# Optimization experiments

Measured on AMD Instinct MI355X. Metric: run time of the kernel, lower is better.

## Reference

```python
import jax, jax.numpy as jnp
import numpy as np

GRID_SIZE = 5
SPLINE_ORDER = 3


def _haar_filters():
    # db1 (Haar) decomposition filters, matching wavelet.create_wavelet_filter:
    # dec_lo[::-1] = [s, s], dec_hi[::-1] = [s, -s]; rec filters are identical for Haar.
    s = np.float32(1.0 / np.sqrt(2.0))
    lo = np.array([s, s], np.float32)
    hi = np.array([s, -s], np.float32)
    # f = a.unsqueeze(0) * b.unsqueeze(1)  ->  f[p, q] = a[q] * b[p]
    def outer(a, b):
        return b[:, None] * a[None, :]
    dec = np.stack([outer(lo, lo), outer(lo, hi), outer(hi, lo), outer(hi, hi)], 0)  # (4,2,2): LL,LH,HL,HH
    return jnp.asarray(dec), jnp.asarray(dec)


def depthwise_conv5(x, w, b):
    # torch Conv2d(C, C, 5, padding='same', groups=C)
    y = jax.lax.conv_general_dilated(
        x, w, window_strides=(1, 1), padding=[(2, 2), (2, 2)],
        dimension_numbers=('NCHW', 'OIHW', 'NCHW'), feature_group_count=x.shape[1])
    return y + b[None, :, None, None]


def kan_linear(x, base_w, spline_w, scaler):
    # efficient-kan KANLinear: base SiLU linear + B-spline linear over last dim.
    in_f = x.shape[-1]
    out_f = base_w.shape[0]
    shp = x.shape
    xf = x.reshape(-1, in_f)                      # (N, in)
    h = 2.0 / GRID_SIZE                           # grid_range [-1, 1]
    grid_1d = jnp.arange(-SPLINE_ORDER, GRID_SIZE + SPLINE_ORDER + 1, dtype=xf.dtype) * h - 1.0
    grid = jnp.broadcast_to(grid_1d, (in_f, grid_1d.shape[0]))  # (in, G+2k+1)
    xe = xf[:, :, None]
    bases = ((xe >= grid[:, :-1]) & (xe < grid[:, 1:])).astype(xf.dtype)
    for k in range(1, SPLINE_ORDER + 1):
        bases = ((xe - grid[:, :-(k + 1)]) / (grid[:, k:-1] - grid[:, :-(k + 1)]) * bases[..., :-1]
                 + (grid[:, k + 1:] - xe) / (grid[:, k + 1:] - grid[:, 1:-k]) * bases[..., 1:])
    # bases: (N, in, G+k)
    base_out = jax.nn.silu(xf) @ base_w.T
    sw = spline_w * scaler[:, :, None]            # scaled_spline_weight (out, in, G+k)
    spline_out = jnp.einsum('nig,oig->no', bases, sw)
    return (base_out + spline_out).reshape(*shp[:-1], out_f)


def setup_inputs() -> dict:
    key = jax.random.key(0)
    ks = jax.random.split(key, 6)
    C, H, W, B = 32, 256, 256, 4
    in_f = C * 4  # 128
    return {
        'x': jax.random.normal(ks[0], (B, C, H, W), jnp.float32),
        'conv_w': jax.random.normal(ks[1], (C, 1, 5, 5), jnp.float32) * 0.2,
        'conv_b': jax.random.normal(ks[2], (C,), jnp.float32) * 0.02,
        'kan_base_w': jax.random.normal(ks[3], (in_f, in_f), jnp.float32) * (1.0 / np.sqrt(in_f)),
        'kan_spline_w': jax.random.normal(ks[4], (in_f, in_f, GRID_SIZE + SPLINE_ORDER), jnp.float32) * 0.1,
        'kan_spline_scaler': 1.0 + 0.1 * jax.random.normal(ks[5], (in_f, in_f), jnp.float32),
    }


def reference(x, conv_w, conv_b, kan_base_w, kan_spline_w, kan_spline_scaler):
    dec, rec = _haar_filters()
    b, c, hh, ww = x.shape
    # Level-1 skip: depthwise base_conv on full-res input
    skip = depthwise_conv5(x, conv_w, conv_b)
    # Haar wavelet transform (stride-2 non-overlapping 2x2 depthwise conv) via reshape+einsum
    x5 = x.reshape(b, c, hh // 2, 2, ww // 2, 2)
    wt = jnp.einsum('bcipjq,kpq->bckij', x5, dec)  # (b, c, 4, h/2, w/2)
    # Subband KAN over last (width) dim of 128 == in_channels*4 -> msi_kan branch
    z = kan_linear(wt, kan_base_w, kan_spline_w, kan_spline_scaler)
    # Inverse wavelet (stride-2 conv_transpose) via einsum scatter
    y = jnp.einsum('bckij,kpq->bcipjq', z, rec).reshape(b, c, hh, ww)
    return y + skip
```

## Files before the change

### kernel.cpp

```cpp
#include <hip/hip_runtime.h>
#include <hip/hip_bf16.h>

using f32x4 = __attribute__((ext_vector_type(4))) float;
using s16x8 = __attribute__((ext_vector_type(8))) short;
using u32x4 = __attribute__((ext_vector_type(4))) unsigned;

constexpr int Bn = 4, Cc = 32, Hh = 256, Ww = 256;
constexpr int H2 = 128, W2 = 128;
constexpr int NF = 128;
constexpr long NROWS = (long)Bn * Cc * 4 * H2;
constexpr int KTOT = 1152;
constexpr int KCH = 288;

__device__ __forceinline__ short f2bf(float f) {
    union { float f; unsigned u; } v; v.f = f;
    unsigned r = v.u + 0x7fffu + ((v.u >> 16) & 1u);
    return (short)(r >> 16);
}

__device__ __forceinline__ unsigned pk_bf16(float a, float b) {
    union { __hip_bfloat162 h; unsigned u; } c;
    c.h.x = __float2bfloat16(a);
    c.h.y = __float2bfloat16(b);
    return c.u;
}

__device__ __forceinline__ void gload_lds16(const void* g, void* l) {
    __builtin_amdgcn_global_load_lds(
        (const __attribute__((address_space(1))) unsigned*)g,
        (__attribute__((address_space(3))) unsigned*)l, 16, 0, 0);
}

__device__ __forceinline__ void window128(float wD, float wC, float wB, float wA,
                                          int ci, unsigned W[4]) {
    unsigned long long P = ((unsigned long long)pk_bf16(wB, wA) << 32)
                         | (unsigned long long)pk_bf16(wD, wC);
    int sh = ci * 16 - 48;
    unsigned long long sl = P << (sh & 63);
    unsigned long long sr = P >> ((-sh) & 63);
    unsigned long long lo = (sh < 0) ? sr : ((sh < 64) ? sl : 0ull);
    int shh = sh - 64;
    unsigned long long sl2 = P << (shh & 63);
    unsigned long long sr2 = P >> ((-shh) & 63);
    unsigned long long hi = (shh >= 0) ? sl2 : (((-shh) < 64) ? sr2 : 0ull);
    W[0] = (unsigned)lo; W[1] = (unsigned)(lo >> 32);
    W[2] = (unsigned)hi; W[3] = (unsigned)(hi >> 32);
}

__global__ __launch_bounds__(256) void k_wbuild(const float* __restrict__ base_w,
                                                const float* __restrict__ spline_w,
                                                const float* __restrict__ scaler,
                                                short* __restrict__ Bg) {
    int idx = blockIdx.x * 256 + threadIdx.x;
    int tile = idx >> 9;
    int r = idx & 511;
    int lane = r >> 3, q = r & 7;
    int ni = tile / 36; int rem = tile - ni * 36;
    int jg = rem / 9;   int ks = rem - jg * 9;
    int o = ni * 16 + (lane & 15);
    int kk = ks * 32 + (lane >> 4) * 8 + q;
    int g = kk >> 5, jl = kk & 31;
    int j = jg * 32 + jl;
    float v = (g == 0) ? base_w[o * NF + j]
                       : spline_w[(long)(o * NF + j) * 8 + (g - 1)] * scaler[o * NF + j];
    Bg[idx] = f2bf(v);
}

__global__ __launch_bounds__(256, 2) void k_fused(const float* __restrict__ x,
                                                  float* __restrict__ z,
                                                  const short* __restrict__ Bg) {
    __shared__ __align__(16) short Bsh[72 * 512];
    const int t = threadIdx.x;
    const int lane = t & 63;
    const int w = t >> 6;
    const int blk = blockIdx.x;
    const int plane = blk >> 2;
    const int band = blk & 3;
    const int i0 = band << 5;
    const int jg0 = blk & 3;
    const int il = lane & 15;
    const int fg = lane >> 4;

    const float sB = (w & 2) ? -1.f : 1.f;
    const float sC = (w & 1) ? -1.f : 1.f;
    const float sD = sB * sC;

    const float* xbase = x + (long)plane * Hh * Ww;
    const float* xr0a = xbase + (long)(2 * (i0 + il)) * Ww;
    const float* xr1a = xr0a + Ww;
    const float* xr0b = xbase + (long)(2 * (i0 + il + 16)) * Ww;
    const float* xr1b = xr0b + Ww;

    f32x4 acc[2][8];
#pragma unroll
    for (int mi = 0; mi < 2; ++mi)
#pragma unroll
        for (int ni = 0; ni < 8; ++ni)
            acc[mi][ni] = (f32x4){0.f, 0.f, 0.f, 0.f};

    for (int j = 0; j < 4; ++j) {
        const int jg = (jg0 + j) & 3;
        const int cb = jg * 64 + fg * 16;

#pragma unroll
        for (int s = 0; s < 18; ++s) {
            int q = s * 4 + w;
            int ni = q / 9, ks = q - ni * 9;
            gload_lds16(&Bg[(long)(((ni * 4 + jg) * 9 + ks) << 9) + lane * 8],
                        &Bsh[q << 9]);
        }

        u32x4 afr[2][9];
#pragma unroll
        for (int mi = 0; mi < 2; ++mi) {
            const float* r0 = mi ? xr0b : xr0a;
            const float* r1 = mi ? xr1b : xr1a;
#pragma unroll
            for (int p = 0; p < 4; ++p) {
                f32x4 va = *(const f32x4*)(r0 + cb + 4 * p);
                f32x4 vb = *(const f32x4*)(r1 + cb + 4 * p);
                float vv[2];
                vv[0] = 0.5f * (va[0] + sB * va[1] + sC * vb[0] + sD * vb[1]);
                vv[1] = 0.5f * (va[2] + sB * va[3] + sC * vb[2] + sD * vb[3]);
                float sl2[2]; unsigned Wf[2][4];
#pragma unroll
                for (int e = 0; e < 2; ++e) {
                    float v = vv[e];
                    float ex = __builtin_amdgcn_exp2f(-1.442695040888963f * v);
                    sl2[e] = v * __builtin_amdgcn_rcpf(1.0f + ex);
                    float xs = __builtin_fmaf(v, 2.5f, 5.5f);
                    xs = fminf(fmaxf(xs, 0.0f), 10.999f);
                    float cf = floorf(xs);
                    float u = xs - cf;
                    int ci = (int)cf;
                    float u2 = u * u, u3 = u2 * u;
                    float wA = u3 * (1.f / 6.f);
                    float wB = (1.f + 3.f * u + 3.f * u2 - 3.f * u3) * (1.f / 6.f);
                    float wC = (4.f - 6.f * u2 + 3.f * u3) * (1.f / 6.f);
                    float um = 1.f - u;
                    float wD = um * um * um * (1.f / 6.f);
                    window128(wD, wC, wB, wA, ci, Wf[e]);
                }
                afr[mi][0][p] = pk_bf16(sl2[0], sl2[1]);
#pragma unroll
                for (int g = 1; g <= 8; ++g) {
                    int wq = (g - 1) >> 1;
                    unsigned sel = ((g - 1) & 1) ? 0x07060302u : 0x05040100u;
                    afr[mi][g][p] = __builtin_amdgcn_perm(Wf[1][wq], Wf[0][wq], sel);
                }
            }
        }

        __syncthreads();

#pragma unroll
        for (int ks = 0; ks < 9; ++ks) {
            s16x8 bfr[8];
#pragma unroll
            for (int ni = 0; ni < 8; ++ni)
                bfr[ni] = *(const s16x8*)&Bsh[((ni * 9 + ks) << 9) + lane * 8];
#pragma unroll
            for (int mi = 0; mi < 2; ++mi) {
                s16x8 a = __builtin_bit_cast(s16x8, afr[mi][ks]);
#pragma unroll
                for (int ni = 0; ni < 8; ++ni)
                    acc[mi][ni] = __builtin_amdgcn_mfma_f32_16x16x32_bf16(
                        a, bfr[ni], acc[mi][ni], 0, 0, 0);
            }
        }
        __syncthreads();
    }

#pragma unroll
    for (int mi = 0; mi < 2; ++mi) {
        long nb = ((long)(plane * 4 + w) * H2 + i0 + mi * 16) * NF;
#pragma unroll
        for (int rr = 0; rr < 4; ++rr) {
            long rowb = nb + (long)(fg * 4 + rr) * NF + il;
#pragma unroll
            for (int ni = 0; ni < 8; ++ni)
                z[rowb + ni * 16] = acc[mi][ni][rr];
        }
    }
}

__global__ __launch_bounds__(256) void k_invconv(const float* __restrict__ x,
                                                 const float* __restrict__ cw,
                                                 const float* __restrict__ cb,
                                                 const float* __restrict__ z,
                                                 float* __restrict__ out) {
    __shared__ float sx[68][70];
    const int t = threadIdx.x;
    const int blk = blockIdx.x;
    const int tile = blk & 15;
    const int plane = blk >> 4;
    const int ty = tile >> 2, tx = tile & 3;
    const int c = plane & 31;
    const int Y0 = ty * 64, X0 = tx * 64;
    const float* xp = x + (long)plane * Hh * Ww;

    for (int idx = t; idx < 68 * 68; idx += 256) {
        int rr = idx / 68, cc2 = idx - rr * 68;
        int yy = Y0 - 2 + rr, xxp = X0 - 2 + cc2;
        float v = 0.f;
        if (yy >= 0 && yy < Hh && xxp >= 0 && xxp < Ww) v = xp[(long)yy * Ww + xxp];
        sx[rr][cc2] = v;
    }
    float w[25];
#pragma unroll
    for (int q = 0; q < 25; ++q) w[q] = cw[c * 25 + q];
    const float bias = cb[c];
    __syncthreads();

    const long zbase = (long)plane * 4 * H2 * W2;
    const long zplane = (long)H2 * W2;
#pragma unroll
    for (int p = 0; p < 4; ++p) {
        int q = t + p * 256;
        int qy = q >> 5, qx = q & 31;
        int i = (Y0 >> 1) + qy, j = (X0 >> 1) + qx;
        long zi = zbase + (long)i * W2 + j;
        float z0 = z[zi];
        float z1 = z[zi + zplane];
        float z2 = z[zi + 2 * zplane];
        float z3 = z[zi + 3 * zplane];
        float y00 = 0.5f * (z0 + z1 + z2 + z3);
        float y01 = 0.5f * (z0 + z1 - z2 - z3);
        float y10 = 0.5f * (z0 - z1 + z2 - z3);
        float y11 = 0.5f * (z0 - z1 - z2 + z3);

        float vals[6][6];
#pragma unroll
        for (int rr = 0; rr < 6; ++rr)
#pragma unroll
            for (int c2 = 0; c2 < 3; ++c2) {
                float2 vv = *(const float2*)&sx[2 * qy + rr][2 * qx + 2 * c2];
                vals[rr][2 * c2] = vv.x; vals[rr][2 * c2 + 1] = vv.y;
            }
        float a00 = bias, a01 = bias, a10 = bias, a11 = bias;
#pragma unroll
        for (int ky = 0; ky < 5; ++ky)
#pragma unroll
            for (int kx = 0; kx < 5; ++kx) {
                float wvv = w[ky * 5 + kx];
                a00 += wvv * vals[ky][kx];
                a01 += wvv * vals[ky][kx + 1];
                a10 += wvv * vals[ky + 1][kx];
                a11 += wvv * vals[ky + 1][kx + 1];
            }
        float* op = out + (long)plane * Hh * Ww + (long)(Y0 + 2 * qy) * Ww + X0 + 2 * qx;
        *(float2*)op = make_float2(a00 + y00, a01 + y01);
        *(float2*)(op + Ww) = make_float2(a10 + y10, a11 + y11);
    }
}

extern "C" void kernel_launch(void* const* d_in, const int* in_sizes, int n_in,
                              void* d_out, int out_size, void* d_ws, size_t ws_size,
                              hipStream_t stream) {
    const float* x        = (const float*)d_in[0];
    const float* conv_w   = (const float*)d_in[1];
    const float* conv_b   = (const float*)d_in[2];
    const float* base_w   = (const float*)d_in[3];
    const float* spline_w = (const float*)d_in[4];
    const float* scaler   = (const float*)d_in[5];
    float* out = (float*)d_out;
    float* z   = (float*)d_ws;
    short* Bg  = (short*)d_out;

    k_wbuild<<<(NF * KTOT) / 256, 256, 0, stream>>>(base_w, spline_w, scaler, Bg);
    k_fused<<<512, 256, 0, stream>>>(x, z, Bg);
    k_invconv<<<Bn * Cc * 16, 256, 0, stream>>>(x, conv_w, conv_b, z, out);
}
```

Measured before the change: 67.49 us.

## Fuse inverse Haar and depthwise conv epilogue into KAN MFMA kernel via LDS

The GEMM kernel now stages its output tile z in shared memory, reusing the B-operand buffer, and directly computes the inverse Haar transform plus the 5x5 depthwise conv and bias, writing the final output. This removes the z round-trip through global memory and one kernel launch. The conv reads x straight from global with a sliding register window instead of an LDS halo tile, and Bg moves to the workspace because out is now written by the same kernel. The fused epilogue adds register pressure under launch_bounds(256,2), and the conv work is tied to the GEMM grid's 512 blocks.

```diff
diff --git a/kernel.cpp b/kernel.cpp
--- a/kernel.cpp
+++ b/kernel.cpp
@@ -8,9 +8,7 @@
 constexpr int Bn = 4, Cc = 32, Hh = 256, Ww = 256;
 constexpr int H2 = 128, W2 = 128;
 constexpr int NF = 128;
-constexpr long NROWS = (long)Bn * Cc * 4 * H2;
 constexpr int KTOT = 1152;
-constexpr int KCH = 288;
 
 __device__ __forceinline__ short f2bf(float f) {
     union { float f; unsigned u; } v; v.f = f;
@@ -66,8 +64,17 @@
     Bg[idx] = f2bf(v);
 }
 
+__device__ __forceinline__ void ldrow6(const float* xrp, int j, bool rok, float o[6]) {
+    float2 lo = (rok && j >= 1)   ? *(const float2*)(xrp + 2 * j - 2) : make_float2(0.f, 0.f);
+    float2 mi = rok               ? *(const float2*)(xrp + 2 * j)     : make_float2(0.f, 0.f);
+    float2 hi = (rok && j <= 126) ? *(const float2*)(xrp + 2 * j + 2) : make_float2(0.f, 0.f);
+    o[0] = lo.x; o[1] = lo.y; o[2] = mi.x; o[3] = mi.y; o[4] = hi.x; o[5] = hi.y;
+}
+
 __global__ __launch_bounds__(256, 2) void k_fused(const float* __restrict__ x,
-                                                  float* __restrict__ z,
+                                                  const float* __restrict__ cw,
+                                                  const float* __restrict__ cb,
+                                                  float* __restrict__ out,
                                                   const short* __restrict__ Bg) {
     __shared__ __align__(16) short Bsh[72 * 512];
     const int t = threadIdx.x;
@@ -100,7 +107,7 @@
 
     for (int j = 0; j < 4; ++j) {
         const int jg = (jg0 + j) & 3;
-        const int cb = jg * 64 + fg * 16;
+        const int cb2 = jg * 64 + fg * 16;
 
 #pragma unroll
         for (int s = 0; s < 18; ++s) {
@@ -117,8 +124,8 @@
             const float* r1 = mi ? xr1b : xr1a;
 #pragma unroll
             for (int p = 0; p < 4; ++p) {
-                f32x4 va = *(const f32x4*)(r0 + cb + 4 * p);
-                f32x4 vb = *(const f32x4*)(r1 + cb + 4 * p);
+                f32x4 va = *(const f32x4*)(r0 + cb2 + 4 * p);
+                f32x4 vb = *(const f32x4*)(r1 + cb2 + 4 * p);
                 float vv[2];
                 vv[0] = 0.5f * (va[0] + sB * va[1] + sC * vb[0] + sD * vb[1]);
                 vv[1] = 0.5f * (va[2] + sB * va[3] + sC * vb[2] + sD * vb[3]);
@@ -171,86 +178,74 @@
         __syncthreads();
     }
 
-#pragma unroll
-    for (int mi = 0; mi < 2; ++mi) {
-        long nb = ((long)(plane * 4 + w) * H2 + i0 + mi * 16) * NF;
-#pragma unroll
-        for (int rr = 0; rr < 4; ++rr) {
-            long rowb = nb + (long)(fg * 4 + rr) * NF + il;
+    constexpr int ZP = 132;
+    float* zsh = (float*)Bsh;
+#pragma unroll
+    for (int mi = 0; mi < 2; ++mi)
+#pragma unroll
+        for (int rr = 0; rr < 4; ++rr)
 #pragma unroll
             for (int ni = 0; ni < 8; ++ni)
-                z[rowb + ni * 16] = acc[mi][ni][rr];
-        }
-    }
-}
-
-__global__ __launch_bounds__(256) void k_invconv(const float* __restrict__ x,
-                                                 const float* __restrict__ cw,
-                                                 const float* __restrict__ cb,
-                                                 const float* __restrict__ z,
-                                                 float* __restrict__ out) {
-    __shared__ float sx[68][70];
-    const int t = threadIdx.x;
-    const int blk = blockIdx.x;
-    const int tile = blk & 15;
-    const int plane = blk >> 4;
-    const int ty = tile >> 2, tx = tile & 3;
+                zsh[(w * 32 + mi * 16 + fg * 4 + rr) * ZP + ni * 16 + il]
+                    = acc[mi][ni][rr];
+    __syncthreads();
+
     const int c = plane & 31;
-    const int Y0 = ty * 64, X0 = tx * 64;
-    const float* xp = x + (long)plane * Hh * Ww;
-
-    for (int idx = t; idx < 68 * 68; idx += 256) {
-        int rr = idx / 68, cc2 = idx - rr * 68;
-        int yy = Y0 - 2 + rr, xxp = X0 - 2 + cc2;
-        float v = 0.f;
-        if (yy >= 0 && yy < Hh && xxp >= 0 && xxp < Ww) v = xp[(long)yy * Ww + xxp];
-        sx[rr][cc2] = v;
-    }
-    float w[25];
-#pragma unroll
-    for (int q = 0; q < 25; ++q) w[q] = cw[c * 25 + q];
+    float cwr[25];
+#pragma unroll
+    for (int q = 0; q < 25; ++q) cwr[q] = cw[c * 25 + q];
     const float bias = cb[c];
-    __syncthreads();
-
-    const long zbase = (long)plane * 4 * H2 * W2;
-    const long zplane = (long)H2 * W2;
-#pragma unroll
-    for (int p = 0; p < 4; ++p) {
-        int q = t + p * 256;
-        int qy = q >> 5, qx = q & 31;
-        int i = (Y0 >> 1) + qy, j = (X0 >> 1) + qx;
-        long zi = zbase + (long)i * W2 + j;
-        float z0 = z[zi];
-        float z1 = z[zi + zplane];
-        float z2 = z[zi + 2 * zplane];
-        float z3 = z[zi + 3 * zplane];
-        float y00 = 0.5f * (z0 + z1 + z2 + z3);
-        float y01 = 0.5f * (z0 + z1 - z2 - z3);
-        float y10 = 0.5f * (z0 - z1 + z2 - z3);
-        float y11 = 0.5f * (z0 - z1 - z2 + z3);
-
-        float vals[6][6];
-#pragma unroll
-        for (int rr = 0; rr < 6; ++rr)
-#pragma unroll
-            for (int c2 = 0; c2 < 3; ++c2) {
-                float2 vv = *(const float2*)&sx[2 * qy + rr][2 * qx + 2 * c2];
-                vals[rr][2 * c2] = vv.x; vals[rr][2 * c2 + 1] = vv.y;
+    float* outp = out + (long)plane * Hh * Ww;
+    const int qyg = t >> 6;
+
+#pragma unroll
+    for (int qxh = 0; qxh < 2; ++qxh) {
+        const int jq = qxh * 64 + lane;
+        float xv[6][6];
+#pragma unroll
+        for (int a = 0; a < 8; ++a) {
+            const int ql = qyg * 8 + a;
+            const int orow = 2 * (i0 + ql);
+            if (a == 0) {
+#pragma unroll
+                for (int r6 = 0; r6 < 6; ++r6) {
+                    int xr = orow - 2 + r6;
+                    ldrow6(xbase + (long)xr * Ww, jq, xr >= 0 && xr < Hh, xv[r6]);
+                }
+            } else {
+#pragma unroll
+                for (int r6 = 0; r6 < 4; ++r6)
+#pragma unroll
+                    for (int c6 = 0; c6 < 6; ++c6) xv[r6][c6] = xv[r6 + 2][c6];
+#pragma unroll
+                for (int r6 = 4; r6 < 6; ++r6) {
+                    int xr = orow - 2 + r6;
+                    ldrow6(xbase + (long)xr * Ww, jq, xr >= 0 && xr < Hh, xv[r6]);
+                }
             }
-        float a00 = bias, a01 = bias, a10 = bias, a11 = bias;
-#pragma unroll
-        for (int ky = 0; ky < 5; ++ky)
-#pragma unroll
-            for (int kx = 0; kx < 5; ++kx) {
-                float wvv = w[ky * 5 + kx];
-                a00 += wvv * vals[ky][kx];
-                a01 += wvv * vals[ky][kx + 1];
-                a10 += wvv * vals[ky + 1][kx];
-                a11 += wvv * vals[ky + 1][kx + 1];
-            }
-        float* op = out + (long)plane * Hh * Ww + (long)(Y0 + 2 * qy) * Ww + X0 + 2 * qx;
-        *(float2*)op = make_float2(a00 + y00, a01 + y01);
-        *(float2*)(op + Ww) = make_float2(a10 + y10, a11 + y11);
+            float z0 = zsh[(ql) * ZP + jq];
+            float z1 = zsh[(32 + ql) * ZP + jq];
+            float z2 = zsh[(64 + ql) * ZP + jq];
+            float z3 = zsh[(96 + ql) * ZP + jq];
+            float y00 = 0.5f * (z0 + z1 + z2 + z3);
+            float y01 = 0.5f * (z0 + z1 - z2 - z3);
+            float y10 = 0.5f * (z0 - z1 + z2 - z3);
+            float y11 = 0.5f * (z0 - z1 - z2 + z3);
+            float s00 = bias, s01 = bias, s10 = bias, s11 = bias;
+#pragma unroll
+            for (int ky = 0; ky < 5; ++ky)
+#pragma unroll
+                for (int kx = 0; kx < 5; ++kx) {
+                    float wv = cwr[ky * 5 + kx];
+                    s00 += wv * xv[ky][kx];
+                    s01 += wv * xv[ky][kx + 1];
+                    s10 += wv * xv[ky + 1][kx];
+                    s11 += wv * xv[ky + 1][kx + 1];
+                }
+            float* op = outp + (long)orow * Ww + 2 * jq;
+            *(float2*)op        = make_float2(s00 + y00, s01 + y01);
+            *(float2*)(op + Ww) = make_float2(s10 + y10, s11 + y11);
+        }
     }
 }
 
@@ -264,10 +259,8 @@
     const float* spline_w = (const float*)d_in[4];
     const float* scaler   = (const float*)d_in[5];
     float* out = (float*)d_out;
-    float* z   = (float*)d_ws;
-    short* Bg  = (short*)d_out;
+    short* Bg  = (short*)d_ws;
 
     k_wbuild<<<(NF * KTOT) / 256, 256, 0, stream>>>(base_w, spline_w, scaler, Bg);
-    k_fused<<<512, 256, 0, stream>>>(x, z, Bg);
-    k_invconv<<<Bn * Cc * 16, 256, 0, stream>>>(x, conv_w, conv_b, z, out);
-}
+    k_fused<<<512, 256, 0, stream>>>(x, conv_w, conv_b, out, Bg);
+}
```

Result: faster. 56.39 us (-16.5%).
